# Performance work log

Measured on AMD Instinct MI355X. Metric: run time of the kernel, lower is better.

Reference implementation:

```python
import jax, jax.numpy as jnp
import numpy as np

OFFSET = 1
NUM_ENTITY = 128

def setup_inputs() -> dict:
    key = jax.random.key(0)
    ks = jax.random.split(key, 8)
    B, L, D = 32, 2048, 1024
    M, E, S = 256, NUM_ENTITY, 128
    H, P = 2048, 512
    return {
        "sequence_output": jax.random.normal(ks[0], (B, L, D), dtype=jnp.float32),
        "mention_pos": jax.random.randint(ks[1], (B, M), 0, L - 2),
        "mention2entity": jnp.sort(jax.random.randint(ks[2], (B, M), 0, E), axis=-1),
        "sent_pos": jax.random.randint(ks[3], (B, S), 0, L - 2),
        "fc1_w": jax.random.normal(ks[4], (D, H), dtype=jnp.float32) * 0.02,
        "fc1_b": jnp.zeros((H,), dtype=jnp.float32),
        "fc2_w": jax.random.normal(ks[5], (H, P), dtype=jnp.float32) * 0.02,
        "fc2_b": jnp.zeros((P,), dtype=jnp.float32),
    }

def _segment_logsumexp(x, seg):
    # x: [M, D] mention embeddings, seg: [M] entity ids -> [E, D]
    m = jax.ops.segment_max(x, seg, num_segments=NUM_ENTITY)           # [E, D]
    m_safe = jnp.where(jnp.isfinite(m), m, 0.0)
    s = jax.ops.segment_sum(jnp.exp(x - m_safe[seg]), seg, num_segments=NUM_ENTITY)
    cnt = jax.ops.segment_sum(jnp.ones((x.shape[0],), x.dtype), seg, num_segments=NUM_ENTITY)
    s_safe = jnp.where(cnt[:, None] > 0, s, 1.0)
    lse = jnp.log(s_safe) + m_safe
    # entities with no mentions stay zero (torch.zeros init in original)
    return jnp.where(cnt[:, None] > 0, lse, 0.0)

def reference(sequence_output, mention_pos, mention2entity, sent_pos, fc1_w, fc1_b, fc2_w, fc2_b):
    # gather mention start-token states (offset = +1 as in self.offset)
    mention_embed = jnp.take_along_axis(
        sequence_output, (mention_pos + OFFSET)[:, :, None], axis=1)  # [B, M, D]
    sent_embed = jnp.take_along_axis(
        sequence_output, (sent_pos + OFFSET)[:, :, None], axis=1)     # [B, S, D]
    entity_embed = jax.vmap(_segment_logsumexp)(mention_embed, mention2entity)  # [B, E, D]
    nodes = jnp.concatenate([mention_embed, entity_embed, sent_embed], axis=1)  # [B, M+E+S, D]
    # projection(): fc1 then fc2 (no nonlinearity, as in the original)
    h = jnp.einsum('bnd,dh->bnh', nodes, fc1_w) + fc1_b
    return jnp.einsum('bnh,hp->bnp', h, fc2_w) + fc2_b
```

## Files before the change

kernel.cpp:

```cpp
#include <hip/hip_runtime.h>
#include <cstdint>

#define DEV __device__ __forceinline__

typedef __attribute__((ext_vector_type(8))) short short8;
typedef __attribute__((ext_vector_type(4))) float f32x4;

DEV unsigned short f2bf(float f) {
    uint32_t u = __builtin_bit_cast(uint32_t, f);
    u += 0x7fffu + ((u >> 16) & 1u);
    return (unsigned short)(u >> 16);
}

DEV uint32_t cvtpk(float a, float b) {
    uint32_t r;
    asm("v_cvt_pk_bf16_f32 %0, %1, %2" : "=v"(r) : "v"(a), "v"(b));
    return r;
}

DEV uint2 pack4(float4 v) {
    uint2 o;
    o.x = cvtpk(v.x, v.y);
    o.y = cvtpk(v.z, v.w);
    return o;
}

DEV void async_copy16(void* lds, const void* g) {
    __builtin_amdgcn_global_load_lds(
        (const __attribute__((address_space(1))) void*)g,
        (__attribute__((address_space(3))) void*)lds, 16, 0, 0);
}

template <int KLEN, int KSTR, int N>
DEV void gemm_body_part(const unsigned short* __restrict__ A,
                        const unsigned short* __restrict__ Bt,
                        float* __restrict__ P,
                        int Mtot, int rowblk, int colblk, int zidx,
                        unsigned short* Al, unsigned short* Bl) {
    int t = threadIdx.x;
    int lane = t & 63, w = t >> 6;
    int wm = w >> 1, wn = w & 1;
    int row0 = rowblk * 128, col0 = colblk * 128;
    size_t kbase = (size_t)zidx * KLEN;
    f32x4 acc[4][4] = {};

    int rifc = lane >> 2;
    int koff = (lane & 3) * 8;
    int c0 = 2 * w, c1 = 2 * w + 1;

    const unsigned short* Abase = A + (size_t)row0 * KSTR + kbase + koff;
    const unsigned short* Bbase = Bt + (size_t)col0 * KSTR + kbase + koff;

    for (int kt = 0; kt < KLEN / 32; ++kt) {
        int k0 = kt * 32;
        __syncthreads();
        async_copy16(&Al[c0 * 512], Abase + (size_t)(c0 * 16 + rifc) * KSTR + k0);
        async_copy16(&Al[c1 * 512], Abase + (size_t)(c1 * 16 + rifc) * KSTR + k0);
        async_copy16(&Bl[c0 * 512], Bbase + (size_t)(c0 * 16 + rifc) * KSTR + k0);
        async_copy16(&Bl[c1 * 512], Bbase + (size_t)(c1 * 16 + rifc) * KSTR + k0);
        __syncthreads();

        int r = lane & 15, kq = lane >> 4;
        short8 a[4], b[4];
        #pragma unroll
        for (int mi = 0; mi < 4; ++mi)
            a[mi] = *reinterpret_cast<const short8*>(&Al[(wm * 64 + mi * 16 + r) * 32 + kq * 8]);
        #pragma unroll
        for (int ni = 0; ni < 4; ++ni)
            b[ni] = *reinterpret_cast<const short8*>(&Bl[(wn * 64 + ni * 16 + r) * 32 + kq * 8]);
        #pragma unroll
        for (int mi = 0; mi < 4; ++mi)
            #pragma unroll
            for (int ni = 0; ni < 4; ++ni)
                acc[mi][ni] = __builtin_amdgcn_mfma_f32_16x16x32_bf16(a[mi], b[ni], acc[mi][ni], 0, 0, 0);
    }

    int r = lane & 15, kq = lane >> 4;
    float* Pz = P + (size_t)zidx * (size_t)N * (size_t)Mtot;
    #pragma unroll
    for (int mi = 0; mi < 4; ++mi)
        #pragma unroll
        for (int ni = 0; ni < 4; ++ni) {
            int col = col0 + wn * 64 + ni * 16 + r;
            #pragma unroll
            for (int j = 0; j < 4; ++j) {
                int row = row0 + wm * 64 + mi * 16 + kq * 4 + j;
                Pz[(size_t)col * Mtot + row] = acc[mi][ni][j];
            }
        }
}

__global__ __launch_bounds__(256) void k_prep(const float* __restrict__ W1,
                                              const float* __restrict__ W2,
                                              const float* __restrict__ b1,
                                              unsigned short* __restrict__ W1c,
                                              unsigned short* __restrict__ W2t,
                                              float* __restrict__ part) {
    __shared__ unsigned short sh[32][33];
    int blk = blockIdx.x, t = threadIdx.x;
    if (blk < 2048) {
        int i = blk * 256 + t;
        float4 v = reinterpret_cast<const float4*>(W1)[i];
        reinterpret_cast<uint2*>(W1c)[i] = pack4(v);
    } else if (blk < 3072) {
        int idx = blk - 2048;
        int h0 = (idx & 63) * 32, p0 = (idx >> 6) * 32;
        int r = t >> 3, c4 = (t & 7) * 4;
        float4 v = *reinterpret_cast<const float4*>(&W2[(size_t)(h0 + r) * 512 + p0 + c4]);
        sh[r][c4 + 0] = f2bf(v.x);
        sh[r][c4 + 1] = f2bf(v.y);
        sh[r][c4 + 2] = f2bf(v.z);
        sh[r][c4 + 3] = f2bf(v.w);
        __syncthreads();
        uint2 o;
        o.x = (uint32_t)sh[c4 + 0][r] | ((uint32_t)sh[c4 + 1][r] << 16);
        o.y = (uint32_t)sh[c4 + 2][r] | ((uint32_t)sh[c4 + 3][r] << 16);
        *reinterpret_cast<uint2*>(&W2t[(size_t)(p0 + r) * 2048 + h0 + c4]) = o;
    } else {
        int hs = blk - 3072;
        float a0 = 0.f, a1 = 0.f;
        #pragma unroll 4
        for (int hh = 0; hh < 32; ++hh) {
            int h = hs * 32 + hh;
            float bb = b1[h];
            a0 += bb * W2[(size_t)h * 512 + t];
            a1 += bb * W2[(size_t)h * 512 + 256 + t];
        }
        part[hs * 512 + t] = a0;
        part[hs * 512 + 256 + t] = a1;
    }
}

__global__ __launch_bounds__(256) void k_mid(const float* __restrict__ seq,
                                             const int* __restrict__ mpos,
                                             const int* __restrict__ m2e,
                                             const unsigned short* __restrict__ W1c,
                                             const unsigned short* __restrict__ W2t,
                                             float* __restrict__ Wpart,
                                             const float* __restrict__ part,
                                             const float* __restrict__ b2,
                                             float* __restrict__ fb,
                                             unsigned short* __restrict__ ent) {
    __shared__ unsigned short Al[128 * 32];
    __shared__ unsigned short Bl[128 * 32];
    __shared__ int sm[256];
    __shared__ int sp[256];
    __shared__ int slo, shi;
    int blk = blockIdx.x, t = threadIdx.x;
    if (blk < 128) {
        gemm_body_part<512, 2048, 512>(W1c, W2t, Wpart, 1024,
                                       (blk >> 2) & 7, blk & 3, blk >> 5, Al, Bl);
    } else if (blk < 130) {
        int p = (blk - 128) * 256 + t;
        float s = b2[p];
        #pragma unroll
        for (int hs = 0; hs < 64; ++hs) s += part[hs * 512 + p];
        fb[p] = s;
    } else {
        int idx = blk - 130;
        int b = idx >> 7, e = idx & 127;
        sm[t] = m2e[b * 256 + t];
        sp[t] = mpos[b * 256 + t] + 1;
        if (t == 0) { slo = 0; shi = 0; }
        __syncthreads();
        if (sm[t] == e && (t == 0 || sm[t - 1] != e)) slo = t;
        if (sm[t] == e && (t == 255 || sm[t + 1] != e)) shi = t + 1;
        __syncthreads();
        int lo = slo, hi = shi;
        float ox, oy, oz, ow;
        if (hi > lo) {
            float s0 = 0.f, s1 = 0.f, s2 = 0.f, s3 = 0.f;
            for (int j = lo; j < hi; ++j) {
                float4 v = *reinterpret_cast<const float4*>(
                    &seq[((size_t)b * 2048 + sp[j]) * 1024 + t * 4]);
                s0 += __expf(v.x); s1 += __expf(v.y);
                s2 += __expf(v.z); s3 += __expf(v.w);
            }
            ox = __logf(s0); oy = __logf(s1);
            oz = __logf(s2); ow = __logf(s3);
        } else {
            ox = oy = oz = ow = 0.f;
        }
        float4 o; o.x = ox; o.y = oy; o.z = oz; o.w = ow;
        *reinterpret_cast<uint2*>(&ent[((size_t)b * 128 + e) * 1024 + t * 4]) = pack4(o);
    }
}

__global__ __launch_bounds__(256) void k_wreduce(const float* __restrict__ P,
                                                 unsigned short* __restrict__ Wt) {
    const size_t SPLIT = 512u * 1024u;
    int i = blockIdx.x * 256 + threadIdx.x;
    float4 a = reinterpret_cast<const float4*>(P)[i];
    float4 b = reinterpret_cast<const float4*>(P + SPLIT)[i];
    float4 c = reinterpret_cast<const float4*>(P + 2 * SPLIT)[i];
    float4 d = reinterpret_cast<const float4*>(P + 3 * SPLIT)[i];
    float4 s;
    s.x = a.x + b.x + c.x + d.x;
    s.y = a.y + b.y + c.y + d.y;
    s.z = a.z + b.z + c.z + d.z;
    s.w = a.w + b.w + c.w + d.w;
    reinterpret_cast<uint2*>(Wt)[i] = pack4(s);
}

__global__ __launch_bounds__(256) void k_gemm_main(const float* __restrict__ seq,
                                                   const int* __restrict__ mpos,
                                                   const int* __restrict__ spos,
                                                   const unsigned short* __restrict__ ent,
                                                   const unsigned short* __restrict__ Wt,
                                                   float* __restrict__ C,
                                                   const float* __restrict__ fb) {
    __shared__ unsigned short Al[128 * 32];
    __shared__ unsigned short Bl[128 * 32];
    int p = blockIdx.x;
    int cpx = gridDim.x >> 3;
    int L = (p & 7) * cpx + (p >> 3);
    int colblk = L & 3;
    int rowblk = L >> 2;

    int t = threadIdx.x;
    int lane = t & 63, w = t >> 6;
    int wm = w >> 1, wn = w & 1;
    int row0 = rowblk * 128, col0 = colblk * 128;
    int b = rowblk >> 2, quad = rowblk & 3;
    f32x4 acc[4][4] = {};

    int rifc = lane >> 2;
    int koff = (lane & 3) * 8;
    int c0 = 2 * w, c1 = 2 * w + 1;
    const unsigned short* Bbase = Wt + (size_t)col0 * 1024 + koff;

    auto compute = [&]() {
        int r = lane & 15, kq = lane >> 4;
        short8 a[4], bfr[4];
        #pragma unroll
        for (int mi = 0; mi < 4; ++mi)
            a[mi] = *reinterpret_cast<const short8*>(&Al[(wm * 64 + mi * 16 + r) * 32 + kq * 8]);
        #pragma unroll
        for (int ni = 0; ni < 4; ++ni)
            bfr[ni] = *reinterpret_cast<const short8*>(&Bl[(wn * 64 + ni * 16 + r) * 32 + kq * 8]);
        #pragma unroll
        for (int mi = 0; mi < 4; ++mi)
            #pragma unroll
            for (int ni = 0; ni < 4; ++ni)
                acc[mi][ni] = __builtin_amdgcn_mfma_f32_16x16x32_bf16(a[mi], bfr[ni], acc[mi][ni], 0, 0, 0);
    };

    auto stageB = [&](int kt) {
        int k0 = kt * 32;
        async_copy16(&Bl[c0 * 512], Bbase + (size_t)(c0 * 16 + rifc) * 1024 + k0);
        async_copy16(&Bl[c1 * 512], Bbase + (size_t)(c1 * 16 + rifc) * 1024 + k0);
    };

    if (quad == 2) {
        const unsigned short* Abase = ent + (size_t)b * 128 * 1024 + koff;
        #pragma unroll 1
        for (int kt = 0; kt < 32; ++kt) {
            int k0 = kt * 32;
            __syncthreads();
            async_copy16(&Al[c0 * 512], Abase + (size_t)(c0 * 16 + rifc) * 1024 + k0);
            async_copy16(&Al[c1 * 512], Abase + (size_t)(c1 * 16 + rifc) * 1024 + k0);
            stageB(kt);
            __syncthreads();
            compute();
        }
    } else {
        int rloc = t >> 3;
        int cof = (t & 7) * 4;
        const float* rp[4];
        {
            int m0, m1, m2, m3;
            if (quad == 3) {
                m0 = spos[b * 128 + rloc] + 1;
                m1 = spos[b * 128 + 32 + rloc] + 1;
                m2 = spos[b * 128 + 64 + rloc] + 1;
                m3 = spos[b * 128 + 96 + rloc] + 1;
            } else {
                int mb = b * 256 + quad * 128;
                m0 = mpos[mb + rloc] + 1;
                m1 = mpos[mb + 32 + rloc] + 1;
                m2 = mpos[mb + 64 + rloc] + 1;
                m3 = mpos[mb + 96 + rloc] + 1;
            }
            rp[0] = seq + ((size_t)b * 2048 + m0) * 1024 + cof;
            rp[1] = seq + ((size_t)b * 2048 + m1) * 1024 + cof;
            rp[2] = seq + ((size_t)b * 2048 + m2) * 1024 + cof;
            rp[3] = seq + ((size_t)b * 2048 + m3) * 1024 + cof;
        }
        float4 va[4];
        auto loadA = [&](int kt, float4* dst) {
            int k0 = kt * 32;
            #pragma unroll
            for (int j = 0; j < 4; ++j)
                dst[j] = *reinterpret_cast<const float4*>(rp[j] + k0);
        };
        auto writeA = [&](const float4* src) {
            #pragma unroll
            for (int j = 0; j < 4; ++j)
                *reinterpret_cast<uint2*>(&Al[(j * 32 + rloc) * 32 + cof]) = pack4(src[j]);
        };
        loadA(0, va);
        #pragma unroll 1
        for (int kt = 0; kt < 32; ++kt) {
            __syncthreads();
            writeA(va);
            stageB(kt);
            __syncthreads();
            float4 vn[4];
            if (kt < 31) loadA(kt + 1, vn);
            compute();
            #pragma unroll
            for (int j = 0; j < 4; ++j) va[j] = vn[j];
        }
    }

    int r = lane & 15, kq = lane >> 4;
    #pragma unroll
    for (int mi = 0; mi < 4; ++mi)
        #pragma unroll
        for (int ni = 0; ni < 4; ++ni) {
            int col = col0 + wn * 64 + ni * 16 + r;
            float bv = fb[col];
            #pragma unroll
            for (int j = 0; j < 4; ++j) {
                int row = row0 + wm * 64 + mi * 16 + kq * 4 + j;
                C[(size_t)row * 512 + col] = acc[mi][ni][j] + bv;
            }
        }
}


extern "C" void kernel_launch(void* const* d_in, const int* in_sizes, int n_in,
                              void* d_out, int out_size, void* d_ws, size_t ws_size,
                              hipStream_t stream) {
    const float* seq  = (const float*)d_in[0];
    const int*   mpos = (const int*)d_in[1];
    const int*   m2e  = (const int*)d_in[2];
    const int*   spos = (const int*)d_in[3];
    const float* W1   = (const float*)d_in[4];
    const float* b1   = (const float*)d_in[5];
    const float* W2   = (const float*)d_in[6];
    const float* b2   = (const float*)d_in[7];
    float* out = (float*)d_out;

    char* ws = (char*)d_ws;
    unsigned short* W1c   = (unsigned short*)(ws);
    unsigned short* W2t   = (unsigned short*)(ws + (4u << 20));
    unsigned short* Wt    = (unsigned short*)(ws + (6u << 20));
    float*          Wpart = (float*)(ws + (8u << 20));
    float*          part  = (float*)(ws + (16u << 20));
    float*          fb    = (float*)(ws + (16u << 20) + (1u << 18));
    unsigned short* ent   = (unsigned short*)(ws + (24u << 20));

    k_prep<<<3136, 256, 0, stream>>>(W1, W2, b1, W1c, W2t, part);
    k_mid<<<4226, 256, 0, stream>>>(seq, mpos, m2e, W1c, W2t, Wpart, part, b2, fb, ent);
    k_wreduce<<<512, 256, 0, stream>>>(Wpart, Wt);
    k_gemm_main<<<512, 256, 0, stream>>>(seq, mpos, spos, ent, Wt, out, fb);
}
```

Measured before the change: 60.79 us.

## Widen main GEMM tile to 128x256 with 512-thread blocks

Doubles the column extent of each GEMM block to 256 and uses 8 waves per block, halving the grid. Each block gathers its A rows (mention/sentence states, converted to bf16) once for twice as many output columns, reducing redundant gathered fp32 reads and conversions. In exchange, the grid shrinks to one block per CU, with fewer independent blocks to hide latency and more LDS per block.

Measured after the change: 68.58 us. 12.8% more time.

```diff
diff --git a/kernel.cpp b/kernel.cpp
--- a/kernel.cpp
+++ b/kernel.cpp
@@ -202,7 +202,7 @@
     reinterpret_cast<uint2*>(Wt)[i] = pack4(s);
 }
 
-__global__ __launch_bounds__(256) void k_gemm_main(const float* __restrict__ seq,
+__global__ __launch_bounds__(512) void k_gemm_main(const float* __restrict__ seq,
                                                    const int* __restrict__ mpos,
                                                    const int* __restrict__ spos,
                                                    const unsigned short* __restrict__ ent,
@@ -210,17 +210,17 @@
                                                    float* __restrict__ C,
                                                    const float* __restrict__ fb) {
     __shared__ unsigned short Al[128 * 32];
-    __shared__ unsigned short Bl[128 * 32];
+    __shared__ unsigned short Bl[256 * 32];
     int p = blockIdx.x;
     int cpx = gridDim.x >> 3;
     int L = (p & 7) * cpx + (p >> 3);
-    int colblk = L & 3;
-    int rowblk = L >> 2;
+    int colblk = L & 1;
+    int rowblk = L >> 1;
 
     int t = threadIdx.x;
     int lane = t & 63, w = t >> 6;
-    int wm = w >> 1, wn = w & 1;
-    int row0 = rowblk * 128, col0 = colblk * 128;
+    int wm = w >> 2, wn = w & 3;
+    int row0 = rowblk * 128, col0 = colblk * 256;
     int b = rowblk >> 2, quad = rowblk & 3;
     f32x4 acc[4][4] = {};
 
@@ -257,46 +257,30 @@
         for (int kt = 0; kt < 32; ++kt) {
             int k0 = kt * 32;
             __syncthreads();
-            async_copy16(&Al[c0 * 512], Abase + (size_t)(c0 * 16 + rifc) * 1024 + k0);
-            async_copy16(&Al[c1 * 512], Abase + (size_t)(c1 * 16 + rifc) * 1024 + k0);
+            async_copy16(&Al[w * 512], Abase + (size_t)(w * 16 + rifc) * 1024 + k0);
             stageB(kt);
             __syncthreads();
             compute();
         }
     } else {
-        int rloc = t >> 3;
-        int cof = (t & 7) * 4;
-        const float* rp[4];
+        int rloc = t >> 2;
+        int cof = (t & 3) * 8;
+        const float* rp;
         {
-            int m0, m1, m2, m3;
-            if (quad == 3) {
-                m0 = spos[b * 128 + rloc] + 1;
-                m1 = spos[b * 128 + 32 + rloc] + 1;
-                m2 = spos[b * 128 + 64 + rloc] + 1;
-                m3 = spos[b * 128 + 96 + rloc] + 1;
-            } else {
-                int mb = b * 256 + quad * 128;
-                m0 = mpos[mb + rloc] + 1;
-                m1 = mpos[mb + 32 + rloc] + 1;
-                m2 = mpos[mb + 64 + rloc] + 1;
-                m3 = mpos[mb + 96 + rloc] + 1;
-            }
-            rp[0] = seq + ((size_t)b * 2048 + m0) * 1024 + cof;
-            rp[1] = seq + ((size_t)b * 2048 + m1) * 1024 + cof;
-            rp[2] = seq + ((size_t)b * 2048 + m2) * 1024 + cof;
-            rp[3] = seq + ((size_t)b * 2048 + m3) * 1024 + cof;
-        }
-        float4 va[4];
+            int pos;
+            if (quad == 3) pos = spos[b * 128 + rloc] + 1;
+            else           pos = mpos[b * 256 + quad * 128 + rloc] + 1;
+            rp = seq + ((size_t)b * 2048 + pos) * 1024 + cof;
+        }
+        float4 va[2];
         auto loadA = [&](int kt, float4* dst) {
             int k0 = kt * 32;
-            #pragma unroll
-            for (int j = 0; j < 4; ++j)
-                dst[j] = *reinterpret_cast<const float4*>(rp[j] + k0);
+            dst[0] = *reinterpret_cast<const float4*>(rp + k0);
+            dst[1] = *reinterpret_cast<const float4*>(rp + k0 + 4);
         };
         auto writeA = [&](const float4* src) {
-            #pragma unroll
-            for (int j = 0; j < 4; ++j)
-                *reinterpret_cast<uint2*>(&Al[(j * 32 + rloc) * 32 + cof]) = pack4(src[j]);
+            *reinterpret_cast<uint2*>(&Al[rloc * 32 + cof])     = pack4(src[0]);
+            *reinterpret_cast<uint2*>(&Al[rloc * 32 + cof + 4]) = pack4(src[1]);
         };
         loadA(0, va);
         #pragma unroll 1
@@ -305,11 +289,10 @@
             writeA(va);
             stageB(kt);
             __syncthreads();
-            float4 vn[4];
+            float4 vn[2];
             if (kt < 31) loadA(kt + 1, vn);
             compute();
-            #pragma unroll
-            for (int j = 0; j < 4; ++j) va[j] = vn[j];
+            va[0] = vn[0]; va[1] = vn[1];
         }
     }
 
@@ -354,5 +337,5 @@
     k_prep<<<3136, 256, 0, stream>>>(W1, W2, b1, W1c, W2t, part);
     k_mid<<<4226, 256, 0, stream>>>(seq, mpos, m2e, W1c, W2t, Wpart, part, b2, fb, ent);
     k_wreduce<<<512, 256, 0, stream>>>(Wpart, Wt);
-    k_gemm_main<<<512, 256, 0, stream>>>(seq, mpos, spos, ent, Wt, out, fb);
-}
+    k_gemm_main<<<256, 512, 0, stream>>>(seq, mpos, spos, ent, Wt, out, fb);
+}
```

## Double-buffer LDS tiles in main GEMM to overlap loads with MFMA

Applied to the files above, without the earlier changes.

Allocates two LDS buffers each for the A and B tiles. The loads for the next k-tile (async B copies, async entity-A copies, or register-staged gathered A) are issued before computing on the current buffer, and each iteration now has one barrier instead of two. The aim is to hide global and LDS load latency behind the MFMA work and to cut synchronisation. In exchange it doubles LDS use per block, which may lower occupancy, and it relies on the barrier to also wait for the async copies to finish.

New measurement: 67.92 us. 1.12x slower.

```diff
diff --git a/kernel.cpp b/kernel.cpp
--- a/kernel.cpp
+++ b/kernel.cpp
@@ -209,8 +209,8 @@
                                                    const unsigned short* __restrict__ Wt,
                                                    float* __restrict__ C,
                                                    const float* __restrict__ fb) {
-    __shared__ unsigned short Al[128 * 32];
-    __shared__ unsigned short Bl[128 * 32];
+    __shared__ unsigned short Al[2][128 * 32];
+    __shared__ unsigned short Bl[2][128 * 32];
     int p = blockIdx.x;
     int cpx = gridDim.x >> 3;
     int L = (p & 7) * cpx + (p >> 3);
@@ -229,15 +229,15 @@
     int c0 = 2 * w, c1 = 2 * w + 1;
     const unsigned short* Bbase = Wt + (size_t)col0 * 1024 + koff;
 
-    auto compute = [&]() {
+    auto compute = [&](int buf) {
         int r = lane & 15, kq = lane >> 4;
         short8 a[4], bfr[4];
         #pragma unroll
         for (int mi = 0; mi < 4; ++mi)
-            a[mi] = *reinterpret_cast<const short8*>(&Al[(wm * 64 + mi * 16 + r) * 32 + kq * 8]);
+            a[mi] = *reinterpret_cast<const short8*>(&Al[buf][(wm * 64 + mi * 16 + r) * 32 + kq * 8]);
         #pragma unroll
         for (int ni = 0; ni < 4; ++ni)
-            bfr[ni] = *reinterpret_cast<const short8*>(&Bl[(wn * 64 + ni * 16 + r) * 32 + kq * 8]);
+            bfr[ni] = *reinterpret_cast<const short8*>(&Bl[buf][(wn * 64 + ni * 16 + r) * 32 + kq * 8]);
         #pragma unroll
         for (int mi = 0; mi < 4; ++mi)
             #pragma unroll
@@ -245,23 +245,27 @@
                 acc[mi][ni] = __builtin_amdgcn_mfma_f32_16x16x32_bf16(a[mi], bfr[ni], acc[mi][ni], 0, 0, 0);
     };
 
-    auto stageB = [&](int kt) {
+    auto stageB = [&](int kt, int buf) {
         int k0 = kt * 32;
-        async_copy16(&Bl[c0 * 512], Bbase + (size_t)(c0 * 16 + rifc) * 1024 + k0);
-        async_copy16(&Bl[c1 * 512], Bbase + (size_t)(c1 * 16 + rifc) * 1024 + k0);
+        async_copy16(&Bl[buf][c0 * 512], Bbase + (size_t)(c0 * 16 + rifc) * 1024 + k0);
+        async_copy16(&Bl[buf][c1 * 512], Bbase + (size_t)(c1 * 16 + rifc) * 1024 + k0);
     };
 
     if (quad == 2) {
         const unsigned short* Abase = ent + (size_t)b * 128 * 1024 + koff;
+        auto stageA = [&](int kt, int buf) {
+            int k0 = kt * 32;
+            async_copy16(&Al[buf][c0 * 512], Abase + (size_t)(c0 * 16 + rifc) * 1024 + k0);
+            async_copy16(&Al[buf][c1 * 512], Abase + (size_t)(c1 * 16 + rifc) * 1024 + k0);
+        };
+        stageA(0, 0); stageB(0, 0);
+        __syncthreads();
         #pragma unroll 1
         for (int kt = 0; kt < 32; ++kt) {
-            int k0 = kt * 32;
+            int cur = kt & 1;
+            if (kt < 31) { stageA(kt + 1, cur ^ 1); stageB(kt + 1, cur ^ 1); }
+            compute(cur);
             __syncthreads();
-            async_copy16(&Al[c0 * 512], Abase + (size_t)(c0 * 16 + rifc) * 1024 + k0);
-            async_copy16(&Al[c1 * 512], Abase + (size_t)(c1 * 16 + rifc) * 1024 + k0);
-            stageB(kt);
-            __syncthreads();
-            compute();
         }
     } else {
         int rloc = t >> 3;
@@ -286,30 +290,32 @@
             rp[2] = seq + ((size_t)b * 2048 + m2) * 1024 + cof;
             rp[3] = seq + ((size_t)b * 2048 + m3) * 1024 + cof;
         }
-        float4 va[4];
+        float4 va[4], vn[4];
         auto loadA = [&](int kt, float4* dst) {
             int k0 = kt * 32;
             #pragma unroll
             for (int j = 0; j < 4; ++j)
                 dst[j] = *reinterpret_cast<const float4*>(rp[j] + k0);
         };
-        auto writeA = [&](const float4* src) {
+        auto writeA = [&](const float4* src, int buf) {
             #pragma unroll
             for (int j = 0; j < 4; ++j)
-                *reinterpret_cast<uint2*>(&Al[(j * 32 + rloc) * 32 + cof]) = pack4(src[j]);
+                *reinterpret_cast<uint2*>(&Al[buf][(j * 32 + rloc) * 32 + cof]) = pack4(src[j]);
         };
         loadA(0, va);
+        stageB(0, 0);
+        writeA(va, 0);
+        __syncthreads();
         #pragma unroll 1
         for (int kt = 0; kt < 32; ++kt) {
+            int cur = kt & 1;
+            if (kt < 31) {
+                loadA(kt + 1, vn);
+                stageB(kt + 1, cur ^ 1);
+            }
+            compute(cur);
+            if (kt < 31) writeA(vn, cur ^ 1);
             __syncthreads();
-            writeA(va);
-            stageB(kt);
-            __syncthreads();
-            float4 vn[4];
-            if (kt < 31) loadA(kt + 1, vn);
-            compute();
-            #pragma unroll
-            for (int j = 0; j < 4; ++j) va[j] = vn[j];
         }
     }
 
```
